# Optimization experiments

Measured on AMD Instinct MI355X. Metric: run time of the kernel, lower is better.

Reference implementation:

```python
import jax, jax.numpy as jnp
import numpy as np

DIM = 4096
N_ITERS = 20
TEMP = 1.0
NOISE_FACTOR = 1.0
EPS = 1e-10


def setup_inputs() -> dict:
    key = jax.random.key(0)
    k1, k2 = jax.random.split(key)
    # logits initialized as log(I + 1e-5) + 0.01*randn, per reset_parameters
    identity = jnp.eye(DIM, dtype=jnp.float32)
    logits = jnp.log(identity + 1e-05) + 0.01 * jax.random.normal(k1, (DIM, DIM), dtype=jnp.float32)
    # uniform noise; Gumbel transform applied inside reference (matches gumbel_noise)
    noise = jax.random.uniform(k2, (DIM, DIM), dtype=jnp.float32)
    return {"logits": logits, "noise": noise}


def reference(logits, noise):
    # Gumbel noise from uniform samples
    g = -jnp.log(-jnp.log(noise + EPS) + EPS) * NOISE_FACTOR
    log_alpha = (logits + g) / TEMP

    def body(la, _):
        la = la - jax.scipy.special.logsumexp(la, axis=1, keepdims=True)  # row normalize
        la = la - jax.scipy.special.logsumexp(la, axis=0, keepdims=True)  # col normalize
        return la, None

    log_alpha, _ = jax.lax.scan(body, log_alpha, None, length=N_ITERS)
    return jnp.exp(log_alpha)
```

## Files before the change

kernel.cpp:

```cpp
#include <hip/hip_runtime.h>
#include <math.h>

#define DIM   4096
#define NITER 20
#define EPSF  1e-10f
#define NB    256
#define NT    1024
#define RPB   16
#define NRG   16

typedef __attribute__((ext_vector_type(4))) unsigned short ushort4_t;

__device__ __forceinline__ float bf2f(unsigned short b) {
    unsigned int x = ((unsigned int)b) << 16;
    return __builtin_bit_cast(float, x);
}
__device__ __forceinline__ unsigned short f2bf(float f) {
    unsigned int x = __builtin_bit_cast(unsigned int, f);
    x += 0x7fffu + ((x >> 16) & 1u);
    return (unsigned short)(x >> 16);
}

__device__ __forceinline__ void st_co(float* p, float v) {
    __hip_atomic_store(p, v, __ATOMIC_RELAXED, __HIP_MEMORY_SCOPE_AGENT);
}
__device__ __forceinline__ float ld_co(const float* p) {
    return __hip_atomic_load(p, __ATOMIC_RELAXED, __HIP_MEMORY_SCOPE_AGENT);
}
__device__ __forceinline__ void st_co2(float* p, float a, float b) {
    unsigned long long v =
        ((unsigned long long)__builtin_bit_cast(unsigned int, b) << 32) |
        (unsigned long long)__builtin_bit_cast(unsigned int, a);
    __hip_atomic_store((unsigned long long*)p, v, __ATOMIC_RELAXED, __HIP_MEMORY_SCOPE_AGENT);
}
__device__ __forceinline__ float2 ld_co2(const float* p) {
    unsigned long long v =
        __hip_atomic_load((const unsigned long long*)p, __ATOMIC_RELAXED, __HIP_MEMORY_SCOPE_AGENT);
    float2 r;
    r.x = __builtin_bit_cast(float, (unsigned int)(v & 0xffffffffull));
    r.y = __builtin_bit_cast(float, (unsigned int)(v >> 32));
    return r;
}

__device__ __forceinline__ void gridbarrier(unsigned* bar, int b, unsigned idx) {
    __syncthreads();
    if (threadIdx.x < 8) {
        const unsigned tgt = 32u * (idx + 1u);
        if (threadIdx.x == 0) {
            __hip_atomic_fetch_add(bar + 32 + 16 * (b & 7), 1u,
                                   __ATOMIC_RELAXED, __HIP_MEMORY_SCOPE_AGENT);
        }
        unsigned* c = bar + 32 + 16 * threadIdx.x;
        while (__hip_atomic_load(c, __ATOMIC_RELAXED, __HIP_MEMORY_SCOPE_AGENT) < tgt)
            __builtin_amdgcn_s_sleep(1);
    }
    __syncthreads();
}

__global__ void zero_bar(unsigned* bar) {
    if (threadIdx.x < 256) bar[threadIdx.x] = 0u;
}

__global__ __launch_bounds__(NT, 4) void sinkhorn_mult(
        const float* __restrict__ logits, const float* __restrict__ noise,
        float* __restrict__ out, float* __restrict__ cg, unsigned* __restrict__ bar) {
    __shared__ unsigned short lm[RPB][DIM];
    __shared__ float          lw[DIM];
    __shared__ float          ru[RPB];

    const int t = threadIdx.x;
    const int b = blockIdx.x;
    const int wave = t >> 6, lane = t & 63;
    const int g0 = b * RPB;
    float* part = out;

#pragma unroll
    for (int r = 0; r < RPB; ++r) {
        const float4 l = *(const float4*)(logits + (size_t)(g0 + r) * DIM + 4 * t);
        const float4 u = *(const float4*)(noise  + (size_t)(g0 + r) * DIM + 4 * t);
        ushort4_t e;
        e.x = f2bf(__expf(l.x) * __builtin_amdgcn_rcpf(EPSF - __logf(u.x + EPSF)));
        e.y = f2bf(__expf(l.y) * __builtin_amdgcn_rcpf(EPSF - __logf(u.y + EPSF)));
        e.z = f2bf(__expf(l.z) * __builtin_amdgcn_rcpf(EPSF - __logf(u.z + EPSF)));
        e.w = f2bf(__expf(l.w) * __builtin_amdgcn_rcpf(EPSF - __logf(u.w + EPSF)));
        *(ushort4_t*)&lm[r][4 * t] = e;
    }
    *(float4*)&lw[4 * t] = make_float4(1.f, 1.f, 1.f, 1.f);
    __syncthreads();

    for (int it = 0; it < NITER; ++it) {
        {
            float4 s4 = make_float4(0.f, 0.f, 0.f, 0.f);
#pragma unroll
            for (int k = 0; k < 16; ++k) {
                const int col = (k * 64 + lane) * 4;
                const ushort4_t e  = *(const ushort4_t*)&lm[wave][col];
                const float4    w4 = *(const float4*)&lw[col];
                s4.x += bf2f(e.x) * w4.x;
                s4.y += bf2f(e.y) * w4.y;
                s4.z += bf2f(e.z) * w4.z;
                s4.w += bf2f(e.w) * w4.w;
            }
            float s = (s4.x + s4.y) + (s4.z + s4.w);
#pragma unroll
            for (int o = 1; o < 64; o <<= 1) s += __shfl_xor(s, o, 64);
            if (lane == 0) ru[wave] = __builtin_amdgcn_rcpf(s);
        }
        __syncthreads();

        {
            float4 p = make_float4(0.f, 0.f, 0.f, 0.f);
#pragma unroll
            for (int r2 = 0; r2 < RPB; ++r2) {
                const ushort4_t e = *(const ushort4_t*)&lm[r2][4 * t];
                const float uu = ru[r2];
                p.x += bf2f(e.x) * uu;
                p.y += bf2f(e.y) * uu;
                p.z += bf2f(e.z) * uu;
                p.w += bf2f(e.w) * uu;
            }
            float* pp = part + (size_t)b * DIM + 4 * t;
            st_co2(pp + 0, p.x, p.y);
            st_co2(pp + 2, p.z, p.w);
        }

        gridbarrier(bar, b, 2u * it);

        {
            const int jj = g0 + wave;
            float s = ld_co(part + (size_t)(lane      ) * DIM + jj)
                    + ld_co(part + (size_t)(lane +  64) * DIM + jj)
                    + ld_co(part + (size_t)(lane + 128) * DIM + jj)
                    + ld_co(part + (size_t)(lane + 192) * DIM + jj);
#pragma unroll
            for (int o = 1; o < 64; o <<= 1) s += __shfl_xor(s, o, 64);
            if (lane == 0) st_co(cg + jj, s);
        }

        gridbarrier(bar, b, 2u * it + 1u);

        {
            const float2 a = ld_co2(cg + 4 * t + 0);
            const float2 c2 = ld_co2(cg + 4 * t + 2);
            lw[4 * t + 0] = __builtin_amdgcn_rcpf(a.x);
            lw[4 * t + 1] = __builtin_amdgcn_rcpf(a.y);
            lw[4 * t + 2] = __builtin_amdgcn_rcpf(c2.x);
            lw[4 * t + 3] = __builtin_amdgcn_rcpf(c2.y);
        }
        __syncthreads();
    }

    const float4 w4 = *(const float4*)&lw[4 * t];
#pragma unroll
    for (int r = 0; r < RPB; ++r) {
        const ushort4_t e = *(const ushort4_t*)&lm[r][4 * t];
        const float uu = ru[r];
        float4 o;
        o.x = bf2f(e.x) * (uu * w4.x);
        o.y = bf2f(e.y) * (uu * w4.y);
        o.z = bf2f(e.z) * (uu * w4.z);
        o.w = bf2f(e.w) * (uu * w4.w);
        *(float4*)(out + (size_t)(g0 + r) * DIM + 4 * t) = o;
    }
}

__device__ __forceinline__ float waveMaxF(float v) {
#pragma unroll
    for (int o = 32; o > 0; o >>= 1) v = fmaxf(v, __shfl_down(v, o, 64));
    return v;
}
__device__ __forceinline__ float waveSumF(float v) {
#pragma unroll
    for (int o = 32; o > 0; o >>= 1) v += __shfl_down(v, o, 64);
    return v;
}

__global__ __launch_bounds__(256) void init_k(const float* __restrict__ logits,
                                              const float* __restrict__ noise,
                                              float* __restrict__ L0,
                                              float* __restrict__ c) {
    int idx = blockIdx.x * blockDim.x + threadIdx.x;
    int stride = gridDim.x * blockDim.x;
    const float4* l4 = (const float4*)logits;
    const float4* n4 = (const float4*)noise;
    float4* o4 = (float4*)L0;
    for (int p = idx; p < DIM * DIM / 4; p += stride) {
        float4 l = l4[p];
        float4 u = n4[p];
        float4 o;
        o.x = l.x - __logf(-__logf(u.x + EPSF) + EPSF);
        o.y = l.y - __logf(-__logf(u.y + EPSF) + EPSF);
        o.z = l.z - __logf(-__logf(u.z + EPSF) + EPSF);
        o.w = l.w - __logf(-__logf(u.w + EPSF) + EPSF);
        o4[p] = o;
    }
    if (idx < DIM) c[idx] = 0.0f;
}

__global__ __launch_bounds__(256) void row_lse(const float* __restrict__ L0,
                                               const float* __restrict__ c,
                                               float* __restrict__ r) {
    __shared__ float red[8];
    const int row = blockIdx.x;
    const int t = threadIdx.x;
    const float4* a4 = (const float4*)(L0 + (size_t)row * DIM);
    const float4* c4 = (const float4*)c;
    float v[16];
    float m = -INFINITY;
#pragma unroll
    for (int k = 0; k < 4; ++k) {
        float4 a  = a4[t + k * 256];
        float4 cc = c4[t + k * 256];
        v[4 * k + 0] = a.x - cc.x;
        v[4 * k + 1] = a.y - cc.y;
        v[4 * k + 2] = a.z - cc.z;
        v[4 * k + 3] = a.w - cc.w;
        m = fmaxf(m, fmaxf(fmaxf(v[4 * k], v[4 * k + 1]), fmaxf(v[4 * k + 2], v[4 * k + 3])));
    }
    m = waveMaxF(m);
    const int lane = t & 63, wid = t >> 6;
    if (lane == 0) red[wid] = m;
    __syncthreads();
    const float bm = fmaxf(fmaxf(red[0], red[1]), fmaxf(red[2], red[3]));
    float s = 0.0f;
#pragma unroll
    for (int q = 0; q < 16; ++q) s += __expf(v[q] - bm);
    s = waveSumF(s);
    if (lane == 0) red[4 + wid] = s;
    __syncthreads();
    if (t == 0) r[row] = bm + __logf(red[4] + red[5] + red[6] + red[7]);
}

__global__ __launch_bounds__(1024) void col_partial(const float* __restrict__ L0,
                                                    const float* __restrict__ r,
                                                    float2* __restrict__ part) {
    __shared__ float sr[256];
    __shared__ float smm[1024];
    __shared__ float sms[1024];
    const int g = blockIdx.x, h = blockIdx.y;
    const int tc = threadIdx.x & 255;
    const int ln = threadIdx.x >> 8;
    if (threadIdx.x < 256) sr[threadIdx.x] = r[h * 256 + threadIdx.x];
    __syncthreads();
    const int j = g * 256 + tc;
    float m = -INFINITY, s = 0.0f;
#pragma unroll 4
    for (int k = 0; k < 64; ++k) {
        int ii = k * 4 + ln;
        float v = L0[(size_t)(h * 256 + ii) * DIM + j] - sr[ii];
        float nm = fmaxf(m, v);
        s = s * __expf(m - nm) + __expf(v - nm);
        m = nm;
    }
    smm[threadIdx.x] = m;
    sms[threadIdx.x] = s;
    __syncthreads();
    if (threadIdx.x < 256) {
        float m0 = smm[tc], m1 = smm[tc + 256], m2 = smm[tc + 512], m3 = smm[tc + 768];
        float M = fmaxf(fmaxf(m0, m1), fmaxf(m2, m3));
        float S = sms[tc] * __expf(m0 - M) + sms[tc + 256] * __expf(m1 - M) +
                  sms[tc + 512] * __expf(m2 - M) + sms[tc + 768] * __expf(m3 - M);
        part[h * DIM + j] = make_float2(M, S);
    }
}

__global__ __launch_bounds__(256) void col_combine(const float2* __restrict__ part,
                                                   float* __restrict__ c) {
    int j = blockIdx.x * 256 + threadIdx.x;
    float pm[NRG], ps[NRG];
    float M = -INFINITY;
#pragma unroll
    for (int h = 0; h < NRG; ++h) {
        float2 p = part[h * DIM + j];
        pm[h] = p.x; ps[h] = p.y;
        M = fmaxf(M, p.x);
    }
    float S = 0.0f;
#pragma unroll
    for (int h = 0; h < NRG; ++h) S += ps[h] * __expf(pm[h] - M);
    c[j] = M + __logf(S);
}

__global__ __launch_bounds__(256) void final_exp(float* __restrict__ L0,
                                                 const float* __restrict__ r,
                                                 const float* __restrict__ c) {
    const float4* c4 = (const float4*)c;
    float4* a4 = (float4*)L0;
    int idx = blockIdx.x * blockDim.x + threadIdx.x;
    int stride = gridDim.x * blockDim.x;
    for (int p = idx; p < DIM * DIM / 4; p += stride) {
        int i  = p >> 10;
        int j4 = p & 1023;
        float4 a = a4[p];
        float rrv = r[i];
        float4 ccv = c4[j4];
        a.x = __expf(a.x - rrv - ccv.x);
        a.y = __expf(a.y - rrv - ccv.y);
        a.z = __expf(a.z - rrv - ccv.z);
        a.w = __expf(a.w - rrv - ccv.w);
        a4[p] = a;
    }
}

extern "C" void kernel_launch(void* const* d_in, const int* in_sizes, int n_in,
                              void* d_out, int out_size, void* d_ws, size_t ws_size,
                              hipStream_t stream) {
    const float* logits = (const float*)d_in[0];
    const float* noise  = (const float*)d_in[1];
    float* out = (float*)d_out;
    float* cg  = (float*)d_ws;
    unsigned* bar = (unsigned*)((char*)d_ws + 16384);

    zero_bar<<<1, 256, 0, stream>>>(bar);
    void* args[] = { (void*)&logits, (void*)&noise, (void*)&out, (void*)&cg, (void*)&bar };
    hipError_t err = hipLaunchCooperativeKernel((const void*)sinkhorn_mult,
                                                dim3(NB), dim3(NT), args, 0, stream);
    if (err != hipSuccess) {
        float* ws = (float*)d_ws;
        float*  r    = ws;
        float*  cf   = ws + DIM;
        float2* part = (float2*)(ws + 2 * DIM);
        init_k<<<4096, 256, 0, stream>>>(logits, noise, out, cf);
        for (int t = 0; t < NITER; ++t) {
            row_lse<<<DIM, 256, 0, stream>>>(out, cf, r);
            col_partial<<<dim3(16, 16), 1024, 0, stream>>>(out, r, part);
            col_combine<<<16, 256, 0, stream>>>(part, cf);
        }
        final_exp<<<4096, 256, 0, stream>>>(out, r, cf);
    }
}
```

Before: 552.1 us.

## Replace grid barriers with tagged per-element dataflow flags in cooperative Sinkhorn

Drops the two grid-wide barriers per iteration. Each partial column sum and each column scale is now stored as a 64-bit word whose high half holds an iteration tag, and consumers spin until the tags of the words they need reach the current iteration. Column reduction is reorganised so each block sums its 16 columns across all 256 partials with a two-level shuffle plus shared-memory reduction, and it publishes the reciprocal directly. The cost is doubled partial-buffer traffic (tags), a separate zeroing kernel that clears 8 MB of the output buffer, and polling on many flags instead of one counter.

Measured after the change: 724.4 us. 31.2% more time.

```diff
diff --git a/kernel.cpp b/kernel.cpp
--- a/kernel.cpp
+++ b/kernel.cpp
@@ -10,6 +10,7 @@
 #define NRG   16
 
 typedef __attribute__((ext_vector_type(4))) unsigned short ushort4_t;
+typedef unsigned long long u64;
 
 __device__ __forceinline__ float bf2f(unsigned short b) {
     unsigned int x = ((unsigned int)b) << 16;
@@ -21,58 +22,38 @@
     return (unsigned short)(x >> 16);
 }
 
-__device__ __forceinline__ void st_co(float* p, float v) {
-    __hip_atomic_store(p, v, __ATOMIC_RELAXED, __HIP_MEMORY_SCOPE_AGENT);
-}
-__device__ __forceinline__ float ld_co(const float* p) {
+__device__ __forceinline__ u64 ld64(const u64* p) {
     return __hip_atomic_load(p, __ATOMIC_RELAXED, __HIP_MEMORY_SCOPE_AGENT);
 }
-__device__ __forceinline__ void st_co2(float* p, float a, float b) {
-    unsigned long long v =
-        ((unsigned long long)__builtin_bit_cast(unsigned int, b) << 32) |
-        (unsigned long long)__builtin_bit_cast(unsigned int, a);
-    __hip_atomic_store((unsigned long long*)p, v, __ATOMIC_RELAXED, __HIP_MEMORY_SCOPE_AGENT);
-}
-__device__ __forceinline__ float2 ld_co2(const float* p) {
-    unsigned long long v =
-        __hip_atomic_load((const unsigned long long*)p, __ATOMIC_RELAXED, __HIP_MEMORY_SCOPE_AGENT);
-    float2 r;
-    r.x = __builtin_bit_cast(float, (unsigned int)(v & 0xffffffffull));
-    r.y = __builtin_bit_cast(float, (unsigned int)(v >> 32));
-    return r;
-}
-
-__device__ __forceinline__ void gridbarrier(unsigned* bar, int b, unsigned idx) {
-    __syncthreads();
-    if (threadIdx.x < 8) {
-        const unsigned tgt = 32u * (idx + 1u);
-        if (threadIdx.x == 0) {
-            __hip_atomic_fetch_add(bar + 32 + 16 * (b & 7), 1u,
-                                   __ATOMIC_RELAXED, __HIP_MEMORY_SCOPE_AGENT);
-        }
-        unsigned* c = bar + 32 + 16 * threadIdx.x;
-        while (__hip_atomic_load(c, __ATOMIC_RELAXED, __HIP_MEMORY_SCOPE_AGENT) < tgt)
-            __builtin_amdgcn_s_sleep(1);
-    }
-    __syncthreads();
-}
-
-__global__ void zero_bar(unsigned* bar) {
-    if (threadIdx.x < 256) bar[threadIdx.x] = 0u;
-}
-
-__global__ __launch_bounds__(NT, 4) void sinkhorn_mult(
+__device__ __forceinline__ void st_tag(u64* p, float v, unsigned tag) {
+    u64 w = ((u64)tag << 32) | (u64)__builtin_bit_cast(unsigned int, v);
+    __hip_atomic_store(p, w, __ATOMIC_RELAXED, __HIP_MEMORY_SCOPE_AGENT);
+}
+__device__ __forceinline__ unsigned tag_of(u64 v) { return (unsigned)(v >> 32); }
+__device__ __forceinline__ float    val_of(u64 v) {
+    return __builtin_bit_cast(float, (unsigned int)(v & 0xffffffffull));
+}
+
+__global__ __launch_bounds__(256) void zero_scratch(u64* part, u64* cgt) {
+    const size_t n = (size_t)NB * DIM;
+    size_t idx = (size_t)blockIdx.x * blockDim.x + threadIdx.x;
+    size_t stride = (size_t)gridDim.x * blockDim.x;
+    for (size_t i = idx; i < n; i += stride) part[i] = 0ull;
+    if (idx < DIM) cgt[idx] = 0ull;
+}
+
+__global__ __launch_bounds__(NT, 4) void sinkhorn_flow(
         const float* __restrict__ logits, const float* __restrict__ noise,
-        float* __restrict__ out, float* __restrict__ cg, unsigned* __restrict__ bar) {
+        float* __restrict__ out, u64* __restrict__ cgt, u64* __restrict__ part) {
     __shared__ unsigned short lm[RPB][DIM];
     __shared__ float          lw[DIM];
     __shared__ float          ru[RPB];
+    __shared__ float4         red[16][4];
 
     const int t = threadIdx.x;
     const int b = blockIdx.x;
     const int wave = t >> 6, lane = t & 63;
     const int g0 = b * RPB;
-    float* part = out;
 
 #pragma unroll
     for (int r = 0; r < RPB; ++r) {
@@ -89,6 +70,8 @@
     __syncthreads();
 
     for (int it = 0; it < NITER; ++it) {
+        const unsigned tg = (unsigned)(it + 1);
+
         {
             float4 s4 = make_float4(0.f, 0.f, 0.f, 0.f);
 #pragma unroll
@@ -119,33 +102,65 @@
                 p.z += bf2f(e.z) * uu;
                 p.w += bf2f(e.w) * uu;
             }
-            float* pp = part + (size_t)b * DIM + 4 * t;
-            st_co2(pp + 0, p.x, p.y);
-            st_co2(pp + 2, p.z, p.w);
-        }
-
-        gridbarrier(bar, b, 2u * it);
+            u64* pp = part + (size_t)b * DIM + 4 * t;
+            st_tag(pp + 0, p.x, tg);
+            st_tag(pp + 1, p.y, tg);
+            st_tag(pp + 2, p.z, tg);
+            st_tag(pp + 3, p.w, tg);
+        }
 
         {
-            const int jj = g0 + wave;
-            float s = ld_co(part + (size_t)(lane      ) * DIM + jj)
-                    + ld_co(part + (size_t)(lane +  64) * DIM + jj)
-                    + ld_co(part + (size_t)(lane + 128) * DIM + jj)
-                    + ld_co(part + (size_t)(lane + 192) * DIM + jj);
-#pragma unroll
-            for (int o = 1; o < 64; o <<= 1) s += __shfl_xor(s, o, 64);
-            if (lane == 0) st_co(cg + jj, s);
-        }
-
-        gridbarrier(bar, b, 2u * it + 1u);
+            const int r = t >> 2, g = t & 3;
+            const u64* q = part + (size_t)r * DIM + 16 * b + 4 * g;
+            u64 v0, v1, v2, v3;
+            for (;;) {
+                v0 = ld64(q + 0); v1 = ld64(q + 1); v2 = ld64(q + 2); v3 = ld64(q + 3);
+                if (tag_of(v0) >= tg && tag_of(v1) >= tg &&
+                    tag_of(v2) >= tg && tag_of(v3) >= tg) break;
+                __builtin_amdgcn_s_sleep(1);
+            }
+            float4 s4 = make_float4(val_of(v0), val_of(v1), val_of(v2), val_of(v3));
+#pragma unroll
+            for (int o = 4; o < 64; o <<= 1) {
+                s4.x += __shfl_xor(s4.x, o, 64);
+                s4.y += __shfl_xor(s4.y, o, 64);
+                s4.z += __shfl_xor(s4.z, o, 64);
+                s4.w += __shfl_xor(s4.w, o, 64);
+            }
+            if (lane < 4) red[wave][lane] = s4;
+        }
+        __syncthreads();
+        if (t < 64) {
+            float4 s4 = red[t >> 2][t & 3];
+#pragma unroll
+            for (int o = 4; o < 64; o <<= 1) {
+                s4.x += __shfl_xor(s4.x, o, 64);
+                s4.y += __shfl_xor(s4.y, o, 64);
+                s4.z += __shfl_xor(s4.z, o, 64);
+                s4.w += __shfl_xor(s4.w, o, 64);
+            }
+            if (t < 4) {
+                u64* cq = cgt + 16 * b + 4 * t;
+                st_tag(cq + 0, __builtin_amdgcn_rcpf(s4.x), tg);
+                st_tag(cq + 1, __builtin_amdgcn_rcpf(s4.y), tg);
+                st_tag(cq + 2, __builtin_amdgcn_rcpf(s4.z), tg);
+                st_tag(cq + 3, __builtin_amdgcn_rcpf(s4.w), tg);
+            }
+        }
 
         {
-            const float2 a = ld_co2(cg + 4 * t + 0);
-            const float2 c2 = ld_co2(cg + 4 * t + 2);
-            lw[4 * t + 0] = __builtin_amdgcn_rcpf(a.x);
-            lw[4 * t + 1] = __builtin_amdgcn_rcpf(a.y);
-            lw[4 * t + 2] = __builtin_amdgcn_rcpf(c2.x);
-            lw[4 * t + 3] = __builtin_amdgcn_rcpf(c2.y);
+            const u64* cq = cgt + 4 * t;
+            u64 v0, v1, v2, v3;
+            for (;;) {
+                v0 = ld64(cq + 0); v1 = ld64(cq + 1); v2 = ld64(cq + 2); v3 = ld64(cq + 3);
+                if (tag_of(v0) >= tg && tag_of(v1) >= tg &&
+                    tag_of(v2) >= tg && tag_of(v3) >= tg) break;
+                __builtin_amdgcn_s_sleep(1);
+            }
+            lw[4 * t + 0] = val_of(v0);
+            lw[4 * t + 1] = val_of(v1);
+            lw[4 * t + 2] = val_of(v2);
+            lw[4 * t + 3] = val_of(v3);
         }
         __syncthreads();
     }
@@ -308,14 +323,19 @@
     const float* logits = (const float*)d_in[0];
     const float* noise  = (const float*)d_in[1];
     float* out = (float*)d_out;
-    float* cg  = (float*)d_ws;
-    unsigned* bar = (unsigned*)((char*)d_ws + 16384);
-
-    zero_bar<<<1, 256, 0, stream>>>(bar);
-    void* args[] = { (void*)&logits, (void*)&noise, (void*)&out, (void*)&cg, (void*)&bar };
-    hipError_t err = hipLaunchCooperativeKernel((const void*)sinkhorn_mult,
-                                                dim3(NB), dim3(NT), args, 0, stream);
-    if (err != hipSuccess) {
+
+    bool tried_flow = false;
+    if (ws_size >= 32768) {
+        u64* cgt  = (u64*)d_ws;
+        u64* part = (u64*)d_out;
+        zero_scratch<<<2048, 256, 0, stream>>>(part, cgt);
+        void* args[] = { (void*)&logits, (void*)&noise, (void*)&out,
+                         (void*)&cgt, (void*)&part };
+        hipError_t err = hipLaunchCooperativeKernel((const void*)sinkhorn_flow,
+                                                    dim3(NB), dim3(NT), args, 0, stream);
+        tried_flow = (err == hipSuccess);
+    }
+    if (!tried_flow) {
         float* ws = (float*)d_ws;
         float*  r    = ws;
         float*  cf   = ws + DIM;
```
